# Kernel optimization log

Measured on AMD Instinct MI355X. Metric: run time of the kernel, lower is better.

## Reference

```python
import jax, jax.numpy as jnp
import numpy as np

N_BLOCKS = 128
B0, B1 = 32, 32
COND_DIM = 0
IN_FEAT = B1 * N_BLOCKS + COND_DIM   # 4096
OUT_FEAT = B0 * N_BLOCKS             # 4096
BATCH = 2048


def _make_masks():
    # block-diagonal mask and strictly-lower block-triangular mask (int32)
    diag = np.kron(np.eye(N_BLOCKS, dtype=np.int32), np.ones((B0, B1), np.int32))
    tril = np.kron(np.tril(np.ones((N_BLOCKS, N_BLOCKS), np.int32), -1),
                   np.ones((B0, B1), np.int32))
    return jnp.asarray(diag), jnp.asarray(tril)


def setup_inputs() -> dict:
    key = jax.random.key(0)
    kx, kw, kb, ks = jax.random.split(key, 4)
    b_diag_mask, b_tril_mask = _make_masks()
    # glorot-like init, masked to the allowed sparsity pattern (as in __init__)
    scale = float(np.sqrt(2.0 / (IN_FEAT + OUT_FEAT)))
    W = jax.random.normal(kw, (OUT_FEAT, IN_FEAT), jnp.float32) * scale
    W = W * (b_diag_mask + b_tril_mask).astype(jnp.float32)
    bias = (jax.random.uniform(kb, (OUT_FEAT,), jnp.float32) - 0.5) * (2.0 / np.sqrt(OUT_FEAT))
    W_log_scale = jnp.log(jax.random.uniform(ks, (OUT_FEAT, 1), jnp.float32, 1e-3, 1.0))
    x = jax.random.normal(kx, (BATCH, IN_FEAT), jnp.float32)
    return {"x": x, "W": W, "bias": bias, "W_log_scale": W_log_scale,
            "b_diag_mask": b_diag_mask, "b_tril_mask": b_tril_mask}


def reference(x, W, bias, W_log_scale, b_diag_mask, b_tril_mask):
    dm = b_diag_mask.astype(W.dtype)
    tm = b_tril_mask.astype(W.dtype)
    # weight normalisation: exp on diag blocks, identity on tril blocks
    Wm = jnp.exp(W) * dm + W * tm
    W_norms = jnp.linalg.norm(Wm, axis=-1, keepdims=True)
    Wn = jnp.exp(W_log_scale) * Wm / W_norms           # (out, in)
    # batched y = Wn @ x + bias (per-sample vector matmul, batched)
    y = jnp.einsum("oi,bi->bo", Wn, x) + bias          # (batch, out)
    # gather diagonal blocks (row-major == jnp.where order in original)
    idx = jnp.arange(N_BLOCKS)
    Wb = Wn[:, COND_DIM:].reshape(N_BLOCKS, B0, N_BLOCKS, B1)
    jac_3d = Wb[idx, :, idx, :]                        # (n_blocks, B0, B1)
    return (y, jnp.log(jac_3d))
```

## Files before the change

kernel.cpp:

```cpp
#include <hip/hip_runtime.h>
#include <hip/hip_bf16.h>

typedef unsigned short u16;
using short8 = __attribute__((ext_vector_type(8))) short;
using f32x4  = __attribute__((ext_vector_type(4))) float;

#define IN_FEAT  4096
#define OUT_FEAT 4096
#define BATCH    2048
#define BPACK    8650752

#define GLOAD16(gp, lp)                                                        \
    __builtin_amdgcn_global_load_lds(                                          \
        (__attribute__((address_space(1))) void*)(gp),                         \
        (__attribute__((address_space(3))) void*)(lp), 16, 0, 0)

__global__ __launch_bounds__(256) void split_x(const float* __restrict__ x,
                                               u16* __restrict__ xhi,
                                               u16* __restrict__ xlo)
{
    const int n4 = (BATCH * IN_FEAT) / 4;
    for (int i = blockIdx.x * blockDim.x + threadIdx.x; i < n4;
         i += gridDim.x * blockDim.x) {
        float4 v = ((const float4*)x)[i];
        float vv[4] = {v.x, v.y, v.z, v.w};
        u16 hh[4], ll[4];
#pragma unroll
        for (int k = 0; k < 4; ++k) {
            __hip_bfloat16 hb = __float2bfloat16(vv[k]);
            float hf = __bfloat162float(hb);
            __hip_bfloat16 lb = __float2bfloat16(vv[k] - hf);
            hh[k] = *(u16*)&hb;
            ll[k] = *(u16*)&lb;
        }
        ushort4 h, l;
        h.x = hh[0]; h.y = hh[1]; h.z = hh[2]; h.w = hh[3];
        l.x = ll[0]; l.y = ll[1]; l.z = ll[2]; l.w = ll[3];
        ((ushort4*)xhi)[i] = h;
        ((ushort4*)xlo)[i] = l;
    }
}

__global__ __launch_bounds__(256) void prep_w(const float* __restrict__ W,
                                              const float* __restrict__ wls,
                                              u16* __restrict__ bhi,
                                              u16* __restrict__ blo,
                                              float* __restrict__ jac)
{
    const int o    = blockIdx.x;
    const int r    = o >> 5;
    const int g    = o >> 7;
    const int kact = (r + 1) * 32;
    const int kpad = (g + 1) << 7;
    const int dlo  = r * 32;

    __shared__ float rowbuf[4096];
    __shared__ float red[4];

    const float* wrow = W + (size_t)o * IN_FEAT;
    float ss = 0.f;
    const int k4 = kact >> 2;
    for (int c4 = threadIdx.x; c4 < k4; c4 += 256) {
        float4 wv = ((const float4*)wrow)[c4];
        float vv[4] = {wv.x, wv.y, wv.z, wv.w};
        const int c = c4 * 4;
#pragma unroll
        for (int e = 0; e < 4; ++e) {
            float wm = (c + e >= dlo) ? expf(vv[e]) : vv[e];
            rowbuf[c + e] = wm;
            ss += wm * wm;
        }
    }
    for (int off = 32; off > 0; off >>= 1) ss += __shfl_down(ss, off, 64);
    const int lane = threadIdx.x & 63, wid = threadIdx.x >> 6;
    if (lane == 0) red[wid] = ss;
    __syncthreads();
    const float total = red[0] + red[1] + red[2] + red[3];
    const float scale = expf(wls[o]) / sqrtf(total);

    const size_t rowbase = (size_t)16384 * ((size_t)g * (g + 1) / 2)
                         + (size_t)(o & 127) * kpad;
    u16* bh = bhi + rowbase;
    u16* bl = blo + rowbase;
    for (int c0 = threadIdx.x * 8; c0 < kpad; c0 += 2048) {
        short8 hv, lv;
#pragma unroll
        for (int e = 0; e < 8; ++e) {
            const int c = c0 + e;
            float wn = (c < kact) ? rowbuf[c] * scale : 0.f;
            __hip_bfloat16 h = __float2bfloat16(wn);
            float hf = __bfloat162float(h);
            __hip_bfloat16 l = __float2bfloat16(wn - hf);
            hv[e] = *(short*)&h;
            lv[e] = *(short*)&l;
            if (c >= dlo && c < kact)
                jac[(size_t)r * 1024 + (size_t)(o & 31) * 32 + (c - dlo)] =
                    logf(wn);
        }
        *(short8*)(bh + c0) = hv;
        *(short8*)(bl + c0) = lv;
    }
}

__global__ __launch_bounds__(256, 2) void gemm_bar(
    const u16* __restrict__ xhi, const u16* __restrict__ xlo,
    const u16* __restrict__ bhi, const u16* __restrict__ blo,
    const float* __restrict__ bias, float* __restrict__ y)
{
    __shared__ __align__(16) u16 As_hi[128][32];
    __shared__ __align__(16) u16 As_lo[128][32];
    __shared__ __align__(16) u16 Bs_hi[128][32];
    __shared__ __align__(16) u16 Bs_lo[128][32];

    const int bid = blockIdx.x;
    const int jj  = bid >> 4;
    const int j   = (jj < 16) ? (31 - jj) : (jj - 16);
    const int i   = bid & 15;
    const int bm0 = i * 128;
    const int bn0 = j * 128;
    const int ksteps = (j + 1) * 4;

    const int tid  = threadIdx.x;
    const int w    = tid >> 6;
    const int lane = tid & 63;
    const int wm   = (w & 1) * 64;
    const int wn   = (w >> 1) * 64;
    const int fr   = lane & 15;
    const int kq   = lane >> 4;
    const int kcg  = (kq ^ ((fr >> 1) & 3)) * 8;
    const int srr  = lane >> 2;
    const int scb  = ((lane & 3) ^ ((lane >> 3) & 3)) * 8;

    const u16* gbase;
    size_t gstride;
    u16* ldst;
    if (w == 0) {
        gbase = xhi + (size_t)bm0 * IN_FEAT; gstride = IN_FEAT;
        ldst  = &As_hi[0][0];
    } else if (w == 1) {
        gbase = xlo + (size_t)bm0 * IN_FEAT; gstride = IN_FEAT;
        ldst  = &As_lo[0][0];
    } else {
        const size_t pbase = (size_t)16384 * ((size_t)j * (j + 1) / 2);
        gstride = (size_t)ksteps * 32;
        if (w == 2) { gbase = bhi + pbase; ldst = &Bs_hi[0][0]; }
        else        { gbase = blo + pbase; ldst = &Bs_lo[0][0]; }
    }

    f32x4 acc[4][4];
#pragma unroll
    for (int a = 0; a < 4; ++a)
#pragma unroll
        for (int b = 0; b < 4; ++b)
            acc[a][b] = (f32x4){0.f, 0.f, 0.f, 0.f};

    for (int kt = 0; kt < ksteps; ++kt) {
        const int kbase = kt * 32;
#pragma unroll
        for (int t = 0; t < 8; ++t) {
            const u16* g = gbase + (size_t)(t * 16 + srr) * gstride
                                 + kbase + scb;
            GLOAD16(g, ldst + t * 16 * 32);
        }
        __syncthreads();

        short8 ah[4], al[4], bh[4], bl[4];
#pragma unroll
        for (int mi = 0; mi < 4; ++mi) {
            const int row = wm + mi * 16 + fr;
            ah[mi] = *(const short8*)(&As_hi[0][0] + row * 32 + kcg);
            al[mi] = *(const short8*)(&As_lo[0][0] + row * 32 + kcg);
        }
#pragma unroll
        for (int ni = 0; ni < 4; ++ni) {
            const int row = wn + ni * 16 + fr;
            bh[ni] = *(const short8*)(&Bs_hi[0][0] + row * 32 + kcg);
            bl[ni] = *(const short8*)(&Bs_lo[0][0] + row * 32 + kcg);
        }
#pragma unroll
        for (int mi = 0; mi < 4; ++mi)
#pragma unroll
            for (int ni = 0; ni < 4; ++ni) {
                f32x4 c = acc[mi][ni];
                c = __builtin_amdgcn_mfma_f32_16x16x32_bf16(ah[mi], bh[ni], c, 0, 0, 0);
                c = __builtin_amdgcn_mfma_f32_16x16x32_bf16(ah[mi], bl[ni], c, 0, 0, 0);
                c = __builtin_amdgcn_mfma_f32_16x16x32_bf16(al[mi], bh[ni], c, 0, 0, 0);
                acc[mi][ni] = c;
            }
        __syncthreads();
    }

    const int crow = (lane >> 4) * 4;
    const int ccol = lane & 15;
#pragma unroll
    for (int ni = 0; ni < 4; ++ni) {
        const int n = bn0 + wn + ni * 16 + ccol;
        const float bv = bias[n];
#pragma unroll
        for (int mi = 0; mi < 4; ++mi) {
#pragma unroll
            for (int q = 0; q < 4; ++q) {
                const int m = bm0 + wm + mi * 16 + crow + q;
                y[(size_t)m * 4096 + n] = acc[mi][ni][q] + bv;
            }
        }
    }
}

extern "C" void kernel_launch(void* const* d_in, const int* in_sizes, int n_in,
                              void* d_out, int out_size, void* d_ws, size_t ws_size,
                              hipStream_t stream)
{
    const float* x    = (const float*)d_in[0];
    const float* W    = (const float*)d_in[1];
    const float* bias = (const float*)d_in[2];
    const float* wls  = (const float*)d_in[3];

    const size_t need = ((size_t)BPACK * 2 + (size_t)BATCH * IN_FEAT * 2)
                        * sizeof(u16);
    if (ws_size < need) return;

    u16* Bhi = (u16*)d_ws;
    u16* Blo = Bhi + (size_t)BPACK;
    u16* Xhi = Blo + (size_t)BPACK;
    u16* Xlo = Xhi + (size_t)BATCH * IN_FEAT;

    float* y   = (float*)d_out;
    float* jac = y + (size_t)BATCH * OUT_FEAT;

    split_x<<<2048, 256, 0, stream>>>(x, Xhi, Xlo);
    prep_w<<<4096, 256, 0, stream>>>(W, wls, Bhi, Blo, jac);
    gemm_bar<<<512, 256, 0, stream>>>(Xhi, Xlo, Bhi, Blo, bias, y);
}
```

Before: 331.6 us.

## Double-buffer GEMM LDS tiles and merge x/W prep into one launch

The GEMM now uses two LDS buffers, so the global-to-LDS load for the next k-step is issued before the MFMAs on the current one, with a single barrier per iteration. The split_x and prep_w kernels are merged into one 6144-block launch, and W rows are processed in reverse order so the longest rows start first. The goal is to hide load latency in the GEMM and to cut one launch plus the tail imbalance. Doubling LDS use (64KB per block) may lower occupancy below the 2 blocks per CU requested by the launch bounds. The merged prep kernel always reserves the 16KB rowbuf, even in the blocks that only split x.

```diff
diff --git a/kernel.cpp b/kernel.cpp
--- a/kernel.cpp
+++ b/kernel.cpp
@@ -15,47 +15,48 @@
         (__attribute__((address_space(1))) void*)(gp),                         \
         (__attribute__((address_space(3))) void*)(lp), 16, 0, 0)
 
-__global__ __launch_bounds__(256) void split_x(const float* __restrict__ x,
-                                               u16* __restrict__ xhi,
-                                               u16* __restrict__ xlo)
+__global__ __launch_bounds__(256) void prep(const float* __restrict__ x,
+                                            const float* __restrict__ W,
+                                            const float* __restrict__ wls,
+                                            u16* __restrict__ xhi,
+                                            u16* __restrict__ xlo,
+                                            u16* __restrict__ bhi,
+                                            u16* __restrict__ blo,
+                                            float* __restrict__ jac)
 {
-    const int n4 = (BATCH * IN_FEAT) / 4;
-    for (int i = blockIdx.x * blockDim.x + threadIdx.x; i < n4;
-         i += gridDim.x * blockDim.x) {
-        float4 v = ((const float4*)x)[i];
-        float vv[4] = {v.x, v.y, v.z, v.w};
-        u16 hh[4], ll[4];
-#pragma unroll
-        for (int k = 0; k < 4; ++k) {
-            __hip_bfloat16 hb = __float2bfloat16(vv[k]);
-            float hf = __bfloat162float(hb);
-            __hip_bfloat16 lb = __float2bfloat16(vv[k] - hf);
-            hh[k] = *(u16*)&hb;
-            ll[k] = *(u16*)&lb;
-        }
-        ushort4 h, l;
-        h.x = hh[0]; h.y = hh[1]; h.z = hh[2]; h.w = hh[3];
-        l.x = ll[0]; l.y = ll[1]; l.z = ll[2]; l.w = ll[3];
-        ((ushort4*)xhi)[i] = h;
-        ((ushort4*)xlo)[i] = l;
-    }
-}
-
-__global__ __launch_bounds__(256) void prep_w(const float* __restrict__ W,
-                                              const float* __restrict__ wls,
-                                              u16* __restrict__ bhi,
-                                              u16* __restrict__ blo,
-                                              float* __restrict__ jac)
-{
-    const int o    = blockIdx.x;
+    __shared__ float rowbuf[4096];
+    __shared__ float red[4];
+
+    if (blockIdx.x >= 4096) {
+        const int bid = blockIdx.x - 4096;
+        const int n4 = (BATCH * IN_FEAT) / 4;
+        for (int i = bid * 256 + threadIdx.x; i < n4; i += 2048 * 256) {
+            float4 v = ((const float4*)x)[i];
+            float vv[4] = {v.x, v.y, v.z, v.w};
+            u16 hh[4], ll[4];
+#pragma unroll
+            for (int k = 0; k < 4; ++k) {
+                __hip_bfloat16 hb = __float2bfloat16(vv[k]);
+                float hf = __bfloat162float(hb);
+                __hip_bfloat16 lb = __float2bfloat16(vv[k] - hf);
+                hh[k] = *(u16*)&hb;
+                ll[k] = *(u16*)&lb;
+            }
+            ushort4 h, l;
+            h.x = hh[0]; h.y = hh[1]; h.z = hh[2]; h.w = hh[3];
+            l.x = ll[0]; l.y = ll[1]; l.z = ll[2]; l.w = ll[3];
+            ((ushort4*)xhi)[i] = h;
+            ((ushort4*)xlo)[i] = l;
+        }
+        return;
+    }
+
+    const int o    = 4095 - blockIdx.x;
     const int r    = o >> 5;
     const int g    = o >> 7;
     const int kact = (r + 1) * 32;
     const int kpad = (g + 1) << 7;
     const int dlo  = r * 32;
-
-    __shared__ float rowbuf[4096];
-    __shared__ float red[4];
 
     const float* wrow = W + (size_t)o * IN_FEAT;
     float ss = 0.f;
@@ -107,10 +108,10 @@
     const u16* __restrict__ bhi, const u16* __restrict__ blo,
     const float* __restrict__ bias, float* __restrict__ y)
 {
-    __shared__ __align__(16) u16 As_hi[128][32];
-    __shared__ __align__(16) u16 As_lo[128][32];
-    __shared__ __align__(16) u16 Bs_hi[128][32];
-    __shared__ __align__(16) u16 Bs_lo[128][32];
+    __shared__ __align__(16) u16 As_hi[2][128][32];
+    __shared__ __align__(16) u16 As_lo[2][128][32];
+    __shared__ __align__(16) u16 Bs_hi[2][128][32];
+    __shared__ __align__(16) u16 Bs_lo[2][128][32];
 
     const int bid = blockIdx.x;
     const int jj  = bid >> 4;
@@ -133,18 +134,18 @@
 
     const u16* gbase;
     size_t gstride;
-    u16* ldst;
+    u16* ldst0;
     if (w == 0) {
         gbase = xhi + (size_t)bm0 * IN_FEAT; gstride = IN_FEAT;
-        ldst  = &As_hi[0][0];
+        ldst0 = &As_hi[0][0][0];
     } else if (w == 1) {
         gbase = xlo + (size_t)bm0 * IN_FEAT; gstride = IN_FEAT;
-        ldst  = &As_lo[0][0];
+        ldst0 = &As_lo[0][0][0];
     } else {
         const size_t pbase = (size_t)16384 * ((size_t)j * (j + 1) / 2);
         gstride = (size_t)ksteps * 32;
-        if (w == 2) { gbase = bhi + pbase; ldst = &Bs_hi[0][0]; }
-        else        { gbase = blo + pbase; ldst = &Bs_lo[0][0]; }
+        if (w == 2) { gbase = bhi + pbase; ldst0 = &Bs_hi[0][0][0]; }
+        else        { gbase = blo + pbase; ldst0 = &Bs_lo[0][0][0]; }
     }
 
     f32x4 acc[4][4];
@@ -154,28 +155,38 @@
         for (int b = 0; b < 4; ++b)
             acc[a][b] = (f32x4){0.f, 0.f, 0.f, 0.f};
 
+#define STAGE(buf, kt)                                                         \
+    do {                                                                       \
+        const int _kb = (kt) * 32;                                             \
+        u16* _dst = ldst0 + (buf) * 4096;                                      \
+        _Pragma("unroll")                                                      \
+        for (int _t = 0; _t < 8; ++_t) {                                       \
+            const u16* _g = gbase + (size_t)(_t * 16 + srr) * gstride          \
+                                  + _kb + scb;                                 \
+            GLOAD16(_g, _dst + _t * 512);                                      \
+        }                                                                      \
+    } while (0)
+
+    STAGE(0, 0);
+    __syncthreads();
+
+    int cur = 0;
     for (int kt = 0; kt < ksteps; ++kt) {
-        const int kbase = kt * 32;
-#pragma unroll
-        for (int t = 0; t < 8; ++t) {
-            const u16* g = gbase + (size_t)(t * 16 + srr) * gstride
-                                 + kbase + scb;
-            GLOAD16(g, ldst + t * 16 * 32);
-        }
-        __syncthreads();
-
+        if (kt + 1 < ksteps) STAGE(cur ^ 1, kt + 1);
+
+        const int cb = cur * 4096;
         short8 ah[4], al[4], bh[4], bl[4];
 #pragma unroll
         for (int mi = 0; mi < 4; ++mi) {
             const int row = wm + mi * 16 + fr;
-            ah[mi] = *(const short8*)(&As_hi[0][0] + row * 32 + kcg);
-            al[mi] = *(const short8*)(&As_lo[0][0] + row * 32 + kcg);
+            ah[mi] = *(const short8*)(&As_hi[0][0][0] + cb + row * 32 + kcg);
+            al[mi] = *(const short8*)(&As_lo[0][0][0] + cb + row * 32 + kcg);
         }
 #pragma unroll
         for (int ni = 0; ni < 4; ++ni) {
             const int row = wn + ni * 16 + fr;
-            bh[ni] = *(const short8*)(&Bs_hi[0][0] + row * 32 + kcg);
-            bl[ni] = *(const short8*)(&Bs_lo[0][0] + row * 32 + kcg);
+            bh[ni] = *(const short8*)(&Bs_hi[0][0][0] + cb + row * 32 + kcg);
+            bl[ni] = *(const short8*)(&Bs_lo[0][0][0] + cb + row * 32 + kcg);
         }
 #pragma unroll
         for (int mi = 0; mi < 4; ++mi)
@@ -188,7 +199,9 @@
                 acc[mi][ni] = c;
             }
         __syncthreads();
-    }
+        cur ^= 1;
+    }
+#undef STAGE
 
     const int crow = (lane >> 4) * 4;
     const int ccol = lane & 15;
@@ -228,7 +241,6 @@
     float* y   = (float*)d_out;
     float* jac = y + (size_t)BATCH * OUT_FEAT;
 
-    split_x<<<2048, 256, 0, stream>>>(x, Xhi, Xlo);
-    prep_w<<<4096, 256, 0, stream>>>(W, wls, Bhi, Blo, jac);
+    prep<<<6144, 256, 0, stream>>>(x, W, wls, Xhi, Xlo, Bhi, Blo, jac);
     gemm_bar<<<512, 256, 0, stream>>>(Xhi, Xlo, Bhi, Blo, bias, y);
 }
```

New measurement: 316.8 us. 4.5% less time.
